# Kernel tuning notes

Hardware: AMD Instinct MI355X
Metric: run time of the kernel (lower is better)

The kernel has to match this reference:

```python
import jax, jax.numpy as jnp
import numpy as np

B, T, L, H = 8, 32, 512, 768  # batch docs, decode steps, encoder length, BART-base hidden


def setup_inputs() -> dict:
    key = jax.random.key(0)
    ks = jax.random.split(key, 7)
    sc = 1.0 / np.sqrt(H).astype(np.float32)
    return {
        "encoder_hn": jax.random.normal(ks[0], (B, L, H), jnp.float32),
        "dec": jax.random.normal(ks[1], (B, T, H), jnp.float32),   # decoder_rnn outputs per step
        "W1": jax.random.normal(ks[2], (H, H), jnp.float32) * sc,  # nnW1 (no bias)
        "W2": jax.random.normal(ks[3], (H, H), jnp.float32) * sc,  # nnW2 (no bias)
        "v": jax.random.normal(ks[4], (H,), jnp.float32) * sc,     # nnV (no bias)
        "starts": jax.random.randint(ks[5], (B, T), 0, 128, jnp.int32),  # ragged slice start per step
        "lens": jax.random.randint(ks[6], (B,), 300, L + 1, jnp.int32),  # curL per document
    }


def reference(encoder_hn, dec, W1, W2, v, starts, lens):
    # pointerLayer batched over (b, t):
    #   WE = nnW1(en)          -> [B, L, H]
    #   WD = nnW2(di expanded) -> [B, T, H]
    #   scores = selu( nnV( selu(WE + WD) ) )  over positions [start, len)
    WE = jnp.einsum('blh,kh->blk', encoder_hn, W1)                 # [B, L, H]
    WD = jnp.einsum('bth,kh->btk', dec, W2)                        # [B, T, H]
    act = jax.nn.selu(WE[:, None, :, :] + WD[:, :, None, :])      # [B, T, L, H]
    scores = jax.nn.selu(jnp.einsum('btlh,h->btl', act, v))       # [B, T, L]
    # ragged slice curencoder_hn[start:curL] expressed as a mask
    pos = jnp.arange(L, dtype=jnp.int32)
    mask = (pos[None, None, :] >= starts[:, :, None]) & \
           (pos[None, None, :] < lens[:, None, None])              # [B, T, L]
    NEG = jnp.asarray(-1e30, scores.dtype)
    logp = jax.nn.log_softmax(jnp.where(mask, scores, NEG), axis=-1)
    return jnp.where(mask, logp, jnp.zeros((), logp.dtype))       # masked log-probs [B, T, L]
```

## Files before the change

kernel.cpp:

```cpp
#include <hip/hip_runtime.h>
#include <math.h>

constexpr int Bn = 8, Tn = 32, Ln = 512, Hn = 768;

typedef __attribute__((ext_vector_type(8))) short bf16x8;
typedef __attribute__((ext_vector_type(4))) float f32x4;

__device__ __forceinline__ short f2bf(float x) {
    unsigned u = __float_as_uint(x);
    u += 0x7FFFu + ((u >> 16) & 1u);
    return (short)(u >> 16);
}
__device__ __forceinline__ float bf2f(unsigned short s) {
    return __uint_as_float(((unsigned)s) << 16);
}

constexpr float kScale = 1.0507009873554804934193349852946f;
constexpr float kAS    = 1.7580993408473768f;

__device__ __forceinline__ float selu(float x) {
    return x > 0.f ? kScale * x : fmaf(kAS, __expf(x), -kAS);
}

__device__ __forceinline__ bf16x8 pack8(float4 a, float4 b) {
    bf16x8 r;
    r[0] = f2bf(a.x); r[1] = f2bf(a.y); r[2] = f2bf(a.z); r[3] = f2bf(a.w);
    r[4] = f2bf(b.x); r[5] = f2bf(b.y); r[6] = f2bf(b.z); r[7] = f2bf(b.w);
    return r;
}

__global__ __launch_bounds__(256) void gemm2_f32_nt(
    const float* __restrict__ A1, const float* __restrict__ B1,
    unsigned short* __restrict__ C1, int M1,
    const float* __restrict__ A2, const float* __restrict__ B2,
    unsigned short* __restrict__ C2,
    int N, int K)
{
    constexpr int BM = 128, BN = 128, BK = 32;
    __shared__ __align__(16) short As[BM * BK];
    __shared__ __align__(16) short Bs[BN * BK];

    const int nblk1 = M1 / BM;
    const int bx = blockIdx.x;
    const float* A; const float* Bm; unsigned short* C; int bm;
    if (bx < nblk1) { A = A1; Bm = B1; C = C1; bm = bx * BM; }
    else            { A = A2; Bm = B2; C = C2; bm = (bx - nblk1) * BM; }
    const int bn = blockIdx.y * BN;

    const int tid  = threadIdx.x;
    const int lane = tid & 63;
    const int wv   = tid >> 6;
    const int quad = lane >> 4;
    const int l16  = lane & 15;
    const int wm   = (wv & 1) * 64;
    const int wn   = (wv >> 1) * 64;

    int srow[2], skk[2];
#pragma unroll
    for (int p = 0; p < 2; ++p) {
        const int unit = tid + (p << 8);
        srow[p] = unit >> 2;
        skk[p]  = (unit & 3) << 3;
    }

    f32x4 acc[4][4] = {};

    float4 cra[2][2], crb[2][2], nra[2][2], nrb[2][2];

    auto gload = [&](float4 ra[2][2], float4 rb[2][2], int k0) {
#pragma unroll
        for (int p = 0; p < 2; ++p) {
            const float* pa = A  + (size_t)(bm + srow[p]) * K + k0 + skk[p];
            ra[p][0] = *(const float4*)pa;
            ra[p][1] = *(const float4*)(pa + 4);
            const float* pb = Bm + (size_t)(bn + srow[p]) * K + k0 + skk[p];
            rb[p][0] = *(const float4*)pb;
            rb[p][1] = *(const float4*)(pb + 4);
        }
    };

    gload(cra, crb, 0);

    for (int k0 = 0; k0 < K; k0 += BK) {
        if (k0 + BK < K) gload(nra, nrb, k0 + BK);
        if (k0 > 0) __syncthreads();
#pragma unroll
        for (int p = 0; p < 2; ++p) {
            const int off = (tid + (p << 8)) << 3;
            *(bf16x8*)&As[off] = pack8(cra[p][0], cra[p][1]);
            *(bf16x8*)&Bs[off] = pack8(crb[p][0], crb[p][1]);
        }
        __syncthreads();

        bf16x8 af[4], bfr[4];
#pragma unroll
        for (int i = 0; i < 4; ++i)
            af[i] = *(const bf16x8*)&As[(wm + i * 16 + l16) * BK + quad * 8];
#pragma unroll
        for (int j = 0; j < 4; ++j)
            bfr[j] = *(const bf16x8*)&Bs[(wn + j * 16 + l16) * BK + quad * 8];
#pragma unroll
        for (int i = 0; i < 4; ++i)
#pragma unroll
            for (int j = 0; j < 4; ++j)
                acc[i][j] = __builtin_amdgcn_mfma_f32_16x16x32_bf16(af[i], bfr[j], acc[i][j], 0, 0, 0);

#pragma unroll
        for (int p = 0; p < 2; ++p) {
            cra[p][0] = nra[p][0]; cra[p][1] = nra[p][1];
            crb[p][0] = nrb[p][0]; crb[p][1] = nrb[p][1];
        }
    }

#pragma unroll
    for (int i = 0; i < 4; ++i)
#pragma unroll
        for (int j = 0; j < 4; ++j)
#pragma unroll
            for (int rr = 0; rr < 4; ++rr) {
                const int row = bm + wm + i * 16 + quad * 4 + rr;
                const int col = bn + wn + j * 16 + l16;
                C[(size_t)row * N + col] = (unsigned short)f2bf(acc[i][j][rr]);
            }
}

__global__ __launch_bounds__(1024) void scores_softmax_fused(
    const unsigned short* __restrict__ WE,
    const unsigned short* __restrict__ WD,
    const float* __restrict__ v,
    const int* __restrict__ starts,
    const int* __restrict__ lens,
    float* __restrict__ out)
{
    const int bid = blockIdx.x;
    const int b = bid & 7;
    const int t = bid >> 3;
    const int bt = b * Tn + t;
    const int tid = threadIdx.x;
    const int lane = tid & 63;
    const int wv = tid >> 6;

    __shared__ float sc[Ln];
    __shared__ float red[16];

    const int start = starts[bt];
    const int len = lens[b];

    float wdr[12], vr[12];
#pragma unroll
    for (int j = 0; j < 3; ++j) {
        const int h = (lane << 2) + (j << 8);
        const ushort4 wdu = *(const ushort4*)(WD + (size_t)bt * Hn + h);
        const float4 vv = *(const float4*)(v + h);
        wdr[j * 4 + 0] = bf2f(wdu.x); wdr[j * 4 + 1] = bf2f(wdu.y);
        wdr[j * 4 + 2] = bf2f(wdu.z); wdr[j * 4 + 3] = bf2f(wdu.w);
        vr[j * 4 + 0] = vv.x; vr[j * 4 + 1] = vv.y;
        vr[j * 4 + 2] = vv.z; vr[j * 4 + 3] = vv.w;
    }

    const unsigned short* WEb = WE + (size_t)b * Ln * Hn;

    for (int k = 0; k < 8; ++k) {
        const int g = wv + (k << 4);
        const int lg = g << 2;
        if (lg + 3 < start || lg >= len) continue;

        ushort4 weu[4][3];
#pragma unroll
        for (int rr = 0; rr < 4; ++rr) {
            const unsigned short* row = WEb + (size_t)(lg + rr) * Hn;
#pragma unroll
            for (int j = 0; j < 3; ++j)
                weu[rr][j] = *(const ushort4*)(row + (lane << 2) + (j << 8));
        }
        float s[4] = {0.f, 0.f, 0.f, 0.f};
#pragma unroll
        for (int j = 0; j < 3; ++j) {
#pragma unroll
            for (int rr = 0; rr < 4; ++rr) {
                float x;
                x = bf2f(weu[rr][j].x) + wdr[j * 4 + 0]; s[rr] = fmaf(selu(x), vr[j * 4 + 0], s[rr]);
                x = bf2f(weu[rr][j].y) + wdr[j * 4 + 1]; s[rr] = fmaf(selu(x), vr[j * 4 + 1], s[rr]);
                x = bf2f(weu[rr][j].z) + wdr[j * 4 + 2]; s[rr] = fmaf(selu(x), vr[j * 4 + 2], s[rr]);
                x = bf2f(weu[rr][j].w) + wdr[j * 4 + 3]; s[rr] = fmaf(selu(x), vr[j * 4 + 3], s[rr]);
            }
        }
#pragma unroll
        for (int off = 32; off > 0; off >>= 1) {
#pragma unroll
            for (int rr = 0; rr < 4; ++rr)
                s[rr] += __shfl_xor(s[rr], off, 64);
        }
        if (lane == 0) {
#pragma unroll
            for (int rr = 0; rr < 4; ++rr)
                sc[lg + rr] = selu(s[rr]);
        }
    }
    __syncthreads();

    const int l = tid;
    const bool active = (l < Ln);
    const bool msk = active && (l >= start) && (l < len);
    const float val = msk ? sc[l] : -1e30f;

    float mx = val;
#pragma unroll
    for (int off = 32; off > 0; off >>= 1)
        mx = fmaxf(mx, __shfl_xor(mx, off, 64));
    if (lane == 0 && wv < 8) red[wv] = mx;
    __syncthreads();
    mx = red[0];
#pragma unroll
    for (int i = 1; i < 8; ++i) mx = fmaxf(mx, red[i]);

    float sm = msk ? __expf(val - mx) : 0.f;
#pragma unroll
    for (int off = 32; off > 0; off >>= 1)
        sm += __shfl_xor(sm, off, 64);
    if (lane == 0 && wv < 8) red[8 + wv] = sm;
    __syncthreads();
    float tot = red[8];
#pragma unroll
    for (int i = 1; i < 8; ++i) tot += red[8 + i];

    if (active) {
        const float logZ = mx + __logf(tot);
        out[(size_t)bt * Ln + l] = msk ? (val - logZ) : 0.f;
    }
}

extern "C" void kernel_launch(void* const* d_in, const int* in_sizes, int n_in,
                              void* d_out, int out_size, void* d_ws, size_t ws_size,
                              hipStream_t stream) {
    const float* enc    = (const float*)d_in[0];
    const float* dec    = (const float*)d_in[1];
    const float* W1     = (const float*)d_in[2];
    const float* W2     = (const float*)d_in[3];
    const float* v      = (const float*)d_in[4];
    const int*   starts = (const int*)d_in[5];
    const int*   lens   = (const int*)d_in[6];
    float* out = (float*)d_out;

    constexpr int n_enc = Bn * Ln * Hn;
    constexpr int n_dec = Bn * Tn * Hn;

    const size_t need = (size_t)(n_enc + n_dec) * 2;
    if (ws_size < need) return;

    unsigned short* WE16 = (unsigned short*)d_ws;
    unsigned short* WD16 = WE16 + n_enc;

    gemm2_f32_nt<<<dim3((Bn * Ln) / 128 + (Bn * Tn) / 128, Hn / 128),
                   dim3(256), 0, stream>>>(
        enc, W1, WE16, Bn * Ln,
        dec, W2, WD16, Hn, Hn);

    scores_softmax_fused<<<dim3(Bn * Tn), dim3(1024), 0, stream>>>(
        WE16, WD16, v, starts, lens, out);
}
```

Baseline: 122.0 us.

## Split fused scores+softmax into a wider-grid scores kernel and a separate softmax

The fused per-(b,t) kernel with 256 blocks of 1024 threads is split into a scores kernel using 1024 blocks of 256 threads, each covering a 128-position chunk of L and exiting early when the chunk lies outside [start, len), plus a separate softmax kernel over a float scores buffer in the workspace. WE rows are now read with 16-byte loads for most of the hidden dimension. The aim is more blocks to fill the CUs and wider loads. The cost is an extra launch and a round trip of the scores through global memory.

```diff
diff --git a/kernel.cpp b/kernel.cpp
--- a/kernel.cpp
+++ b/kernel.cpp
@@ -64,7 +64,6 @@
     }
 
     f32x4 acc[4][4] = {};
-
     float4 cra[2][2], crb[2][2], nra[2][2], nrb[2][2];
 
     auto gload = [&](float4 ra[2][2], float4 rb[2][2], int k0) {
@@ -124,91 +123,117 @@
             }
 }
 
-__global__ __launch_bounds__(1024) void scores_softmax_fused(
+__global__ __launch_bounds__(256) void scores_kernel(
     const unsigned short* __restrict__ WE,
     const unsigned short* __restrict__ WD,
     const float* __restrict__ v,
     const int* __restrict__ starts,
     const int* __restrict__ lens,
-    float* __restrict__ out)
+    float* __restrict__ sc)
 {
     const int bid = blockIdx.x;
     const int b = bid & 7;
-    const int t = bid >> 3;
+    const int r = bid >> 3;
+    const int t = r & 31;
+    const int q = r >> 5;
     const int bt = b * Tn + t;
+    const int lane = threadIdx.x & 63;
+    const int wv = threadIdx.x >> 6;
+
+    const int start = starts[bt];
+    const int len = lens[b];
+    const int lbase = q * 128;
+    if (lbase + 127 < start || lbase >= len) return;
+
+    const int h8 = lane << 3;
+    const int h4 = 512 + (lane << 2);
+    float wd8[8], v8[8], wd4[4], v4[4];
+    {
+        const bf16x8 wdu8 = *(const bf16x8*)(WD + (size_t)bt * Hn + h8);
+        const ushort4 wdu4 = *(const ushort4*)(WD + (size_t)bt * Hn + h4);
+#pragma unroll
+        for (int e = 0; e < 8; ++e) { wd8[e] = bf2f((unsigned short)wdu8[e]); v8[e] = v[h8 + e]; }
+        wd4[0] = bf2f(wdu4.x); wd4[1] = bf2f(wdu4.y);
+        wd4[2] = bf2f(wdu4.z); wd4[3] = bf2f(wdu4.w);
+        const float4 vv = *(const float4*)(v + h4);
+        v4[0] = vv.x; v4[1] = vv.y; v4[2] = vv.z; v4[3] = vv.w;
+    }
+
+    const unsigned short* WEb = WE + (size_t)b * Ln * Hn;
+
+    for (int k = 0; k < 8; ++k) {
+        const int g = wv + (k << 2);
+        const int lg = lbase + (g << 2);
+        if (lg + 3 < start || lg >= len) continue;
+
+        bf16x8 w8[4]; ushort4 w4[4];
+#pragma unroll
+        for (int rr = 0; rr < 4; ++rr) {
+            const unsigned short* row = WEb + (size_t)(lg + rr) * Hn;
+            w8[rr] = *(const bf16x8*)(row + h8);
+            w4[rr] = *(const ushort4*)(row + h4);
+        }
+        float s[4] = {0.f, 0.f, 0.f, 0.f};
+#pragma unroll
+        for (int e = 0; e < 8; ++e) {
+#pragma unroll
+            for (int rr = 0; rr < 4; ++rr) {
+                const float x = bf2f((unsigned short)w8[rr][e]) + wd8[e];
+                s[rr] = fmaf(selu(x), v8[e], s[rr]);
+            }
+        }
+        {
+            const unsigned short c4[4][4] = {
+                {w4[0].x, w4[0].y, w4[0].z, w4[0].w},
+                {w4[1].x, w4[1].y, w4[1].z, w4[1].w},
+                {w4[2].x, w4[2].y, w4[2].z, w4[2].w},
+                {w4[3].x, w4[3].y, w4[3].z, w4[3].w}};
+#pragma unroll
+            for (int e = 0; e < 4; ++e)
+#pragma unroll
+                for (int rr = 0; rr < 4; ++rr) {
+                    const float x = bf2f(c4[rr][e]) + wd4[e];
+                    s[rr] = fmaf(selu(x), v4[e], s[rr]);
+                }
+        }
+#pragma unroll
+        for (int off = 32; off > 0; off >>= 1) {
+#pragma unroll
+            for (int rr = 0; rr < 4; ++rr)
+                s[rr] += __shfl_xor(s[rr], off, 64);
+        }
+        if (lane == 0) {
+#pragma unroll
+            for (int rr = 0; rr < 4; ++rr)
+                sc[(size_t)bt * Ln + lg + rr] = selu(s[rr]);
+        }
+    }
+}
+
+__global__ __launch_bounds__(512) void softmax_kernel(
+    const float* __restrict__ sc,
+    const int* __restrict__ starts,
+    const int* __restrict__ lens,
+    float* __restrict__ out)
+{
+    __shared__ float red[16];
+    const int bt = blockIdx.x;
+    const int b = bt / Tn;
     const int tid = threadIdx.x;
     const int lane = tid & 63;
     const int wv = tid >> 6;
 
-    __shared__ float sc[Ln];
-    __shared__ float red[16];
-
     const int start = starts[bt];
     const int len = lens[b];
-
-    float wdr[12], vr[12];
-#pragma unroll
-    for (int j = 0; j < 3; ++j) {
-        const int h = (lane << 2) + (j << 8);
-        const ushort4 wdu = *(const ushort4*)(WD + (size_t)bt * Hn + h);
-        const float4 vv = *(const float4*)(v + h);
-        wdr[j * 4 + 0] = bf2f(wdu.x); wdr[j * 4 + 1] = bf2f(wdu.y);
-        wdr[j * 4 + 2] = bf2f(wdu.z); wdr[j * 4 + 3] = bf2f(wdu.w);
-        vr[j * 4 + 0] = vv.x; vr[j * 4 + 1] = vv.y;
-        vr[j * 4 + 2] = vv.z; vr[j * 4 + 3] = vv.w;
-    }
-
-    const unsigned short* WEb = WE + (size_t)b * Ln * Hn;
-
-    for (int k = 0; k < 8; ++k) {
-        const int g = wv + (k << 4);
-        const int lg = g << 2;
-        if (lg + 3 < start || lg >= len) continue;
-
-        ushort4 weu[4][3];
-#pragma unroll
-        for (int rr = 0; rr < 4; ++rr) {
-            const unsigned short* row = WEb + (size_t)(lg + rr) * Hn;
-#pragma unroll
-            for (int j = 0; j < 3; ++j)
-                weu[rr][j] = *(const ushort4*)(row + (lane << 2) + (j << 8));
-        }
-        float s[4] = {0.f, 0.f, 0.f, 0.f};
-#pragma unroll
-        for (int j = 0; j < 3; ++j) {
-#pragma unroll
-            for (int rr = 0; rr < 4; ++rr) {
-                float x;
-                x = bf2f(weu[rr][j].x) + wdr[j * 4 + 0]; s[rr] = fmaf(selu(x), vr[j * 4 + 0], s[rr]);
-                x = bf2f(weu[rr][j].y) + wdr[j * 4 + 1]; s[rr] = fmaf(selu(x), vr[j * 4 + 1], s[rr]);
-                x = bf2f(weu[rr][j].z) + wdr[j * 4 + 2]; s[rr] = fmaf(selu(x), vr[j * 4 + 2], s[rr]);
-                x = bf2f(weu[rr][j].w) + wdr[j * 4 + 3]; s[rr] = fmaf(selu(x), vr[j * 4 + 3], s[rr]);
-            }
-        }
-#pragma unroll
-        for (int off = 32; off > 0; off >>= 1) {
-#pragma unroll
-            for (int rr = 0; rr < 4; ++rr)
-                s[rr] += __shfl_xor(s[rr], off, 64);
-        }
-        if (lane == 0) {
-#pragma unroll
-            for (int rr = 0; rr < 4; ++rr)
-                sc[lg + rr] = selu(s[rr]);
-        }
-    }
-    __syncthreads();
-
     const int l = tid;
-    const bool active = (l < Ln);
-    const bool msk = active && (l >= start) && (l < len);
-    const float val = msk ? sc[l] : -1e30f;
+    const bool msk = (l >= start) && (l < len);
+    const float val = msk ? sc[(size_t)bt * Ln + l] : -1e30f;
 
     float mx = val;
 #pragma unroll
     for (int off = 32; off > 0; off >>= 1)
         mx = fmaxf(mx, __shfl_xor(mx, off, 64));
-    if (lane == 0 && wv < 8) red[wv] = mx;
+    if (lane == 0) red[wv] = mx;
     __syncthreads();
     mx = red[0];
 #pragma unroll
@@ -218,16 +243,14 @@
 #pragma unroll
     for (int off = 32; off > 0; off >>= 1)
         sm += __shfl_xor(sm, off, 64);
-    if (lane == 0 && wv < 8) red[8 + wv] = sm;
+    if (lane == 0) red[8 + wv] = sm;
     __syncthreads();
     float tot = red[8];
 #pragma unroll
     for (int i = 1; i < 8; ++i) tot += red[8 + i];
 
-    if (active) {
-        const float logZ = mx + __logf(tot);
-        out[(size_t)bt * Ln + l] = msk ? (val - logZ) : 0.f;
-    }
+    const float logZ = mx + __logf(tot);
+    out[(size_t)bt * Ln + l] = msk ? (val - logZ) : 0.f;
 }
 
 extern "C" void kernel_launch(void* const* d_in, const int* in_sizes, int n_in,
@@ -244,18 +267,22 @@
 
     constexpr int n_enc = Bn * Ln * Hn;
     constexpr int n_dec = Bn * Tn * Hn;
-
-    const size_t need = (size_t)(n_enc + n_dec) * 2;
+    constexpr int n_sc  = Bn * Tn * Ln;
+
+    const size_t need = (size_t)(n_enc + n_dec) * 2 + (size_t)n_sc * 4;
     if (ws_size < need) return;
 
     unsigned short* WE16 = (unsigned short*)d_ws;
     unsigned short* WD16 = WE16 + n_enc;
+    float* sc = (float*)(WD16 + n_dec);
 
     gemm2_f32_nt<<<dim3((Bn * Ln) / 128 + (Bn * Tn) / 128, Hn / 128),
                    dim3(256), 0, stream>>>(
         enc, W1, WE16, Bn * Ln,
         dec, W2, WD16, Hn, Hn);
 
-    scores_softmax_fused<<<dim3(Bn * Tn), dim3(1024), 0, stream>>>(
-        WE16, WD16, v, starts, lens, out);
-}
+    scores_kernel<<<dim3(1024), dim3(256), 0, stream>>>(
+        WE16, WD16, v, starts, lens, sc);
+    softmax_kernel<<<dim3(Bn * Tn), dim3(512), 0, stream>>>(
+        sc, starts, lens, out);
+}
```

Result: slower. 124.6 us (+2.1%).
